# Kernel optimization log

Hardware: AMD Instinct MI355X
Metric: run time of the kernel (lower is better)

The kernel has to match this reference:

```python
import jax, jax.numpy as jnp
import numpy as np

EPS = 1e-8

def setup_inputs() -> dict:
    key = jax.random.key(0)
    k0, k1, k2, k3, k4 = jax.random.split(key, 5)
    B, N, K, Q, L, F = 8, 5, 5, 4, 128, 768
    support_emb = jax.random.normal(k0, (B, N, K, L, F), dtype=jnp.float32)
    query_emb = jax.random.normal(k1, (B, N * Q, L, F), dtype=jnp.float32)
    B_mask = jax.random.randint(k2, (B, N, K, L), 0, 2, dtype=jnp.int32)
    I_mask = jax.random.randint(k3, (B, N, K, L), 0, 2, dtype=jnp.int32)
    trigger_label = jax.random.randint(k4, (B, N * Q, L), 0, 2 * N + 1, dtype=jnp.int32)
    return {"support_emb": support_emb, "query_emb": query_emb, "B_mask": B_mask,
            "I_mask": I_mask, "trigger_label": trigger_label, "N": N, "K": K, "Q": Q}

def _proto(support_emb, Bm, Im, N):
    # support_emb: (B,N,K,L,F); Bm/Im: (B,N,K,L) float
    sum_B = jnp.einsum('bnklf,bnkl->bnf', support_emb, Bm)
    cnt_B = Bm.sum((2, 3))[..., None] + EPS
    pB = sum_B / cnt_B                                   # (B,N,F)
    sum_I = jnp.einsum('bnklf,bnkl->bnf', support_emb, Im)
    cnt_I = Im.sum((2, 3))[..., None] + EPS
    pI = sum_I / cnt_I                                   # (B,N,F)
    Om = 1.0 - Bm - Im                                   # (B,N,K,L)
    sum_O = jnp.einsum('bnklf,bnkl->bf', support_emb, Om)
    cnt_O = Om.sum((1, 2, 3))[:, None] + EPS
    pO = sum_O / cnt_O                                   # (B,F)
    Bsz, F = pO.shape
    # interleave: tags [O, B_0, I_0, B_1, I_1, ...]
    pBI = jnp.stack([pB, pI], axis=2).reshape(Bsz, 2 * N, F)
    return jnp.concatenate([pO[:, None, :], pBI], axis=1)  # (B, 2N+1, F)

def reference(support_emb, query_emb, B_mask, I_mask, trigger_label, N, K, Q):
    dt = support_emb.dtype
    Bm = B_mask.astype(dt)
    Im = I_mask.astype(dt)
    prototype = _proto(support_emb, Bm, Im, N)             # (B, 2N+1, F)
    # similarity: broadcast dot product -> batched GEMM
    logits = jnp.einsum('bqlf,btf->bqlt', query_emb, prototype)  # (B, NQ, L, 2N+1)
    T = logits.shape[-1]
    flat = logits.reshape(-1, T)
    pred = jnp.argmax(flat, axis=1)
    lab = trigger_label.reshape(-1)
    logp = jax.nn.log_softmax(flat, axis=-1)
    loss = -jnp.take_along_axis(logp, lab[:, None], axis=1).mean()
    return (loss, logits, pred)
```

## Files before the change

### kernel.cpp

```cpp
#include <hip/hip_runtime.h>
#include <cstdint>
#include <cstddef>

#define EPS 1e-8f

#define Bsz 8
#define Nn  5
#define Kk  5
#define Qq  4
#define Ll  128
#define Ff  768
#define NQ  (Nn*Qq)
#define Tt  (2*Nn+1)
#define KL  (Kk*Ll)
#define ROWS_PER_B (NQ*Ll)
#define NROWS (Bsz*ROWS_PER_B)
#define F4  (Ff/4)
#define BN  (Bsz*Nn)

#define S1_CHUNK 32
#define S1_CH    (KL / S1_CHUNK)

__global__ __launch_bounds__(256) void stage1_partials(
    const float* __restrict__ sup,
    const int*   __restrict__ Bm,
    const int*   __restrict__ Im,
    float* __restrict__ accum,
    float* __restrict__ cnt)
{
    int blk  = blockIdx.x;
    int bn   = blk / S1_CH;
    int ch   = blk - bn * S1_CH;
    int pos0 = ch * S1_CHUNK;
    int tid  = threadIdx.x;

    const float* sp = sup + ((size_t)bn * KL + pos0) * Ff;
    const int*   bp = Bm + bn * KL + pos0;
    const int*   ip = Im + bn * KL + pos0;

    __shared__ float smB[S1_CHUNK];
    __shared__ float smI[S1_CHUNK];
    if (tid < S1_CHUNK) {
        smB[tid] = (float)bp[tid];
        smI[tid] = (float)ip[tid];
    }
    __syncthreads();

    float aB0=0,aB1=0,aB2=0, aI0=0,aI1=0,aI2=0, aO0=0,aO1=0,aO2=0;
    const float* r = sp + tid;
    #pragma unroll 4
    for (int p = 0; p < S1_CHUNK; ++p, r += Ff) {
        float mb = smB[p], mi = smI[p];
        float mo = 1.0f - mb - mi;
        float v0 = r[0], v1 = r[256], v2 = r[512];
        aB0 = fmaf(mb, v0, aB0); aB1 = fmaf(mb, v1, aB1); aB2 = fmaf(mb, v2, aB2);
        aI0 = fmaf(mi, v0, aI0); aI1 = fmaf(mi, v1, aI1); aI2 = fmaf(mi, v2, aI2);
        aO0 = fmaf(mo, v0, aO0); aO1 = fmaf(mo, v1, aO1); aO2 = fmaf(mo, v2, aO2);
    }
    float* o = accum + (size_t)bn * (3 * Ff);
    atomicAdd(&o[tid],            aB0); atomicAdd(&o[tid + 256],          aB1); atomicAdd(&o[tid + 512],          aB2);
    atomicAdd(&o[Ff + tid],       aI0); atomicAdd(&o[Ff + tid + 256],     aI1); atomicAdd(&o[Ff + tid + 512],     aI2);
    atomicAdd(&o[2*Ff + tid],     aO0); atomicAdd(&o[2*Ff + tid + 256],   aO1); atomicAdd(&o[2*Ff + tid + 512],   aO2);

    if (tid == 0) { float c = 0; for (int p = 0; p < S1_CHUNK; ++p) c += smB[p]; atomicAdd(&cnt[bn*2],   c); }
    if (tid == 1) { float c = 0; for (int p = 0; p < S1_CHUNK; ++p) c += smI[p]; atomicAdd(&cnt[bn*2+1], c); }
}

__global__ void stage2_proto(
    const float* __restrict__ accum,
    const float* __restrict__ cnt,
    float* __restrict__ proto)
{
    int b = blockIdx.x;
    int f = threadIdx.x;

    float sumO = 0.0f, cntO = 0.0f;
    #pragma unroll
    for (int n = 0; n < Nn; ++n) {
        int bn = b * Nn + n;
        const float* a = accum + (size_t)bn * (3 * Ff);
        float cB = cnt[bn*2], cI = cnt[bn*2+1];
        proto[((size_t)b * Tt + (1 + 2 * n)) * Ff + f] = a[f]        / (cB + EPS);
        proto[((size_t)b * Tt + (2 + 2 * n)) * Ff + f] = a[Ff + f]   / (cI + EPS);
        sumO += a[2*Ff + f];
        cntO += (float)KL - cB - cI;
    }
    proto[(size_t)b * Tt * Ff + f] = sumO / (cntO + EPS);
}

#define S3_BLOCKS_PER_B 160
#define S3_ROWS_PER_WAVE 4

__global__ __launch_bounds__(256) void stage3_logits(
    const float* __restrict__ query,
    const float* __restrict__ proto,
    const int*   __restrict__ label,
    float* __restrict__ out_logits,
    float* __restrict__ out_pred,
    float* __restrict__ loss_out)
{
    __shared__ float sLoss;

    int b  = blockIdx.x / S3_BLOCKS_PER_B;
    int rg = blockIdx.x - b * S3_BLOCKS_PER_B;
    int wave = threadIdx.x >> 6;
    int lane = threadIdx.x & 63;

    if (threadIdx.x == 0) sLoss = 0.0f;
    __syncthreads();

    const float4* pg = (const float4*)(proto + (size_t)b * Tt * Ff);
    float4 P[Tt][3];
    #pragma unroll
    for (int t = 0; t < Tt; ++t) {
        P[t][0] = pg[t * F4 + lane];
        P[t][1] = pg[t * F4 + 64 + lane];
        P[t][2] = pg[t * F4 + 128 + lane];
    }

    int row0 = rg * (4 * S3_ROWS_PER_WAVE) + wave * S3_ROWS_PER_WAVE;
    float wloss = 0.0f;

    for (int r = 0; r < S3_ROWS_PER_WAVE; ++r) {
        size_t grow = (size_t)b * ROWS_PER_B + row0 + r;
        const float4* q = (const float4*)(query + grow * Ff);
        float4 q0 = q[lane], q1 = q[64 + lane], q2 = q[128 + lane];
        int lab = label[grow];

        float acc[Tt];
        #pragma unroll
        for (int t = 0; t < Tt; ++t) {
            float d;
            d = q0.x * P[t][0].x;
            d = fmaf(q0.y, P[t][0].y, d); d = fmaf(q0.z, P[t][0].z, d); d = fmaf(q0.w, P[t][0].w, d);
            d = fmaf(q1.x, P[t][1].x, d); d = fmaf(q1.y, P[t][1].y, d);
            d = fmaf(q1.z, P[t][1].z, d); d = fmaf(q1.w, P[t][1].w, d);
            d = fmaf(q2.x, P[t][2].x, d); d = fmaf(q2.y, P[t][2].y, d);
            d = fmaf(q2.z, P[t][2].z, d); d = fmaf(q2.w, P[t][2].w, d);
            acc[t] = d;
        }
        #pragma unroll
        for (int off = 32; off > 0; off >>= 1) {
            #pragma unroll
            for (int t = 0; t < Tt; ++t) acc[t] += __shfl_xor(acc[t], off, 64);
        }
        float m = acc[0]; int bt = 0;
        #pragma unroll
        for (int t = 1; t < Tt; ++t) if (acc[t] > m) { m = acc[t]; bt = t; }
        float s = 0.0f;
        #pragma unroll
        for (int t = 0; t < Tt; ++t) s += __expf(acc[t] - m);
        float labv = acc[0];
        #pragma unroll
        for (int t = 1; t < Tt; ++t) labv = (lab == t) ? acc[t] : labv;
        float myv = acc[0];
        #pragma unroll
        for (int t = 1; t < Tt; ++t) myv = (lane == t) ? acc[t] : myv;

        if (lane < Tt) out_logits[grow * Tt + lane] = myv;
        if (lane == 0) out_pred[grow] = (float)bt;
        wloss += (m + __logf(s)) - labv;
    }

    if (lane == 0) atomicAdd(&sLoss, wloss);
    __syncthreads();
    if (threadIdx.x == 0) atomicAdd(loss_out, sLoss * (1.0f / (float)NROWS));
}

extern "C" void kernel_launch(void* const* d_in, const int* in_sizes, int n_in,
                              void* d_out, int out_size, void* d_ws, size_t ws_size,
                              hipStream_t stream) {
    const float* sup   = (const float*)d_in[0];
    const float* query = (const float*)d_in[1];
    const int*   Bm    = (const int*)d_in[2];
    const int*   Im    = (const int*)d_in[3];
    const int*   lab   = (const int*)d_in[4];

    float* w     = (float*)d_ws;
    float* accum = w;
    float* cnt   = accum + (size_t)BN * 3 * Ff;
    float* proto = cnt + 2 * BN;
    size_t zeroBytes = ((size_t)BN * 3 * Ff + 2 * BN) * sizeof(float);

    float* loss_out   = (float*)d_out;
    float* out_logits = (float*)d_out + 1;
    float* out_pred   = (float*)d_out + 1 + (size_t)NROWS * Tt;

    hipMemsetAsync(d_ws, 0, zeroBytes, stream);
    hipMemsetAsync(d_out, 0, sizeof(float), stream);

    stage1_partials<<<BN * S1_CH, 256, 0, stream>>>(sup, Bm, Im, accum, cnt);
    stage2_proto<<<Bsz, Ff, 0, stream>>>(accum, cnt, proto);
    stage3_logits<<<Bsz * S3_BLOCKS_PER_B, 256, 0, stream>>>(query, proto, lab,
                                                             out_logits, out_pred, loss_out);
}
```

Measured before the change: 208.8 us.

## Fuse prototype normalization into logits kernel and vectorize support accumulation

Removes the separate stage2 prototype kernel. Each stage3 block now rebuilds its batch's prototypes in registers from the raw accumulators and counts, scaling by reciprocals. Stage1 switches to 192 threads with one float4 load per row instead of three strided scalar loads. This drops one kernel launch and the proto round trip through memory, at the cost of every stage3 block redundantly reading about 46KB of accumulators and doing the normalization again.

```diff
diff --git a/kernel.cpp b/kernel.cpp
--- a/kernel.cpp
+++ b/kernel.cpp
@@ -21,7 +21,7 @@
 #define S1_CHUNK 32
 #define S1_CH    (KL / S1_CHUNK)
 
-__global__ __launch_bounds__(256) void stage1_partials(
+__global__ __launch_bounds__(192) void stage1_partials(
     const float* __restrict__ sup,
     const int*   __restrict__ Bm,
     const int*   __restrict__ Im,
@@ -34,9 +34,9 @@
     int pos0 = ch * S1_CHUNK;
     int tid  = threadIdx.x;
 
-    const float* sp = sup + ((size_t)bn * KL + pos0) * Ff;
-    const int*   bp = Bm + bn * KL + pos0;
-    const int*   ip = Im + bn * KL + pos0;
+    const float4* sp = (const float4*)(sup + ((size_t)bn * KL + pos0) * Ff);
+    const int*    bp = Bm + bn * KL + pos0;
+    const int*    ip = Im + bn * KL + pos0;
 
     __shared__ float smB[S1_CHUNK];
     __shared__ float smI[S1_CHUNK];
@@ -46,46 +46,25 @@
     }
     __syncthreads();
 
-    float aB0=0,aB1=0,aB2=0, aI0=0,aI1=0,aI2=0, aO0=0,aO1=0,aO2=0;
-    const float* r = sp + tid;
+    float aBx=0,aBy=0,aBz=0,aBw=0, aIx=0,aIy=0,aIz=0,aIw=0, aOx=0,aOy=0,aOz=0,aOw=0;
+    const float4* r = sp + tid;
     #pragma unroll 4
-    for (int p = 0; p < S1_CHUNK; ++p, r += Ff) {
+    for (int p = 0; p < S1_CHUNK; ++p, r += F4) {
         float mb = smB[p], mi = smI[p];
         float mo = 1.0f - mb - mi;
-        float v0 = r[0], v1 = r[256], v2 = r[512];
-        aB0 = fmaf(mb, v0, aB0); aB1 = fmaf(mb, v1, aB1); aB2 = fmaf(mb, v2, aB2);
-        aI0 = fmaf(mi, v0, aI0); aI1 = fmaf(mi, v1, aI1); aI2 = fmaf(mi, v2, aI2);
-        aO0 = fmaf(mo, v0, aO0); aO1 = fmaf(mo, v1, aO1); aO2 = fmaf(mo, v2, aO2);
+        float4 v = *r;
+        aBx = fmaf(mb, v.x, aBx); aBy = fmaf(mb, v.y, aBy); aBz = fmaf(mb, v.z, aBz); aBw = fmaf(mb, v.w, aBw);
+        aIx = fmaf(mi, v.x, aIx); aIy = fmaf(mi, v.y, aIy); aIz = fmaf(mi, v.z, aIz); aIw = fmaf(mi, v.w, aIw);
+        aOx = fmaf(mo, v.x, aOx); aOy = fmaf(mo, v.y, aOy); aOz = fmaf(mo, v.z, aOz); aOw = fmaf(mo, v.w, aOw);
     }
     float* o = accum + (size_t)bn * (3 * Ff);
-    atomicAdd(&o[tid],            aB0); atomicAdd(&o[tid + 256],          aB1); atomicAdd(&o[tid + 512],          aB2);
-    atomicAdd(&o[Ff + tid],       aI0); atomicAdd(&o[Ff + tid + 256],     aI1); atomicAdd(&o[Ff + tid + 512],     aI2);
-    atomicAdd(&o[2*Ff + tid],     aO0); atomicAdd(&o[2*Ff + tid + 256],   aO1); atomicAdd(&o[2*Ff + tid + 512],   aO2);
+    int c = 4 * tid;
+    atomicAdd(&o[c],   aBx); atomicAdd(&o[c+1],   aBy); atomicAdd(&o[c+2],   aBz); atomicAdd(&o[c+3],   aBw);
+    atomicAdd(&o[Ff+c],aIx); atomicAdd(&o[Ff+c+1],aIy); atomicAdd(&o[Ff+c+2],aIz); atomicAdd(&o[Ff+c+3],aIw);
+    atomicAdd(&o[2*Ff+c],aOx); atomicAdd(&o[2*Ff+c+1],aOy); atomicAdd(&o[2*Ff+c+2],aOz); atomicAdd(&o[2*Ff+c+3],aOw);
 
-    if (tid == 0) { float c = 0; for (int p = 0; p < S1_CHUNK; ++p) c += smB[p]; atomicAdd(&cnt[bn*2],   c); }
-    if (tid == 1) { float c = 0; for (int p = 0; p < S1_CHUNK; ++p) c += smI[p]; atomicAdd(&cnt[bn*2+1], c); }
-}
-
-__global__ void stage2_proto(
-    const float* __restrict__ accum,
-    const float* __restrict__ cnt,
-    float* __restrict__ proto)
-{
-    int b = blockIdx.x;
-    int f = threadIdx.x;
-
-    float sumO = 0.0f, cntO = 0.0f;
-    #pragma unroll
-    for (int n = 0; n < Nn; ++n) {
-        int bn = b * Nn + n;
-        const float* a = accum + (size_t)bn * (3 * Ff);
-        float cB = cnt[bn*2], cI = cnt[bn*2+1];
-        proto[((size_t)b * Tt + (1 + 2 * n)) * Ff + f] = a[f]        / (cB + EPS);
-        proto[((size_t)b * Tt + (2 + 2 * n)) * Ff + f] = a[Ff + f]   / (cI + EPS);
-        sumO += a[2*Ff + f];
-        cntO += (float)KL - cB - cI;
-    }
-    proto[(size_t)b * Tt * Ff + f] = sumO / (cntO + EPS);
+    if (tid == 0) { float s = 0; for (int p = 0; p < S1_CHUNK; ++p) s += smB[p]; atomicAdd(&cnt[bn*2],   s); }
+    if (tid == 1) { float s = 0; for (int p = 0; p < S1_CHUNK; ++p) s += smI[p]; atomicAdd(&cnt[bn*2+1], s); }
 }
 
 #define S3_BLOCKS_PER_B 160
@@ -93,7 +72,8 @@
 
 __global__ __launch_bounds__(256) void stage3_logits(
     const float* __restrict__ query,
-    const float* __restrict__ proto,
+    const float* __restrict__ accum,
+    const float* __restrict__ cnt,
     const int*   __restrict__ label,
     float* __restrict__ out_logits,
     float* __restrict__ out_pred,
@@ -109,14 +89,33 @@
     if (threadIdx.x == 0) sLoss = 0.0f;
     __syncthreads();
 
-    const float4* pg = (const float4*)(proto + (size_t)b * Tt * Ff);
     float4 P[Tt][3];
+    float4 o0, o1, o2;
+    o0.x=o0.y=o0.z=o0.w=0; o1=o0; o2=o0;
+    float sumCB = 0.0f, sumCI = 0.0f;
     #pragma unroll
-    for (int t = 0; t < Tt; ++t) {
-        P[t][0] = pg[t * F4 + lane];
-        P[t][1] = pg[t * F4 + 64 + lane];
-        P[t][2] = pg[t * F4 + 128 + lane];
+    for (int n = 0; n < Nn; ++n) {
+        int bn = b * Nn + n;
+        const float4* a = (const float4*)(accum + (size_t)bn * (3 * Ff));
+        float cB = cnt[2*bn], cI = cnt[2*bn+1];
+        float sB = 1.0f / (cB + EPS);
+        float sI = 1.0f / (cI + EPS);
+        float4 v;
+        v = a[lane];            P[1+2*n][0].x=v.x*sB; P[1+2*n][0].y=v.y*sB; P[1+2*n][0].z=v.z*sB; P[1+2*n][0].w=v.w*sB;
+        v = a[64+lane];         P[1+2*n][1].x=v.x*sB; P[1+2*n][1].y=v.y*sB; P[1+2*n][1].z=v.z*sB; P[1+2*n][1].w=v.w*sB;
+        v = a[128+lane];        P[1+2*n][2].x=v.x*sB; P[1+2*n][2].y=v.y*sB; P[1+2*n][2].z=v.z*sB; P[1+2*n][2].w=v.w*sB;
+        v = a[192+lane];        P[2+2*n][0].x=v.x*sI; P[2+2*n][0].y=v.y*sI; P[2+2*n][0].z=v.z*sI; P[2+2*n][0].w=v.w*sI;
+        v = a[256+lane];        P[2+2*n][1].x=v.x*sI; P[2+2*n][1].y=v.y*sI; P[2+2*n][1].z=v.z*sI; P[2+2*n][1].w=v.w*sI;
+        v = a[320+lane];        P[2+2*n][2].x=v.x*sI; P[2+2*n][2].y=v.y*sI; P[2+2*n][2].z=v.z*sI; P[2+2*n][2].w=v.w*sI;
+        v = a[384+lane];        o0.x+=v.x; o0.y+=v.y; o0.z+=v.z; o0.w+=v.w;
+        v = a[448+lane];        o1.x+=v.x; o1.y+=v.y; o1.z+=v.z; o1.w+=v.w;
+        v = a[512+lane];        o2.x+=v.x; o2.y+=v.y; o2.z+=v.z; o2.w+=v.w;
+        sumCB += cB; sumCI += cI;
     }
+    float sO = 1.0f / ((float)(KL * Nn) - sumCB - sumCI + EPS);
+    P[0][0].x=o0.x*sO; P[0][0].y=o0.y*sO; P[0][0].z=o0.z*sO; P[0][0].w=o0.w*sO;
+    P[0][1].x=o1.x*sO; P[0][1].y=o1.y*sO; P[0][1].z=o1.z*sO; P[0][1].w=o1.w*sO;
+    P[0][2].x=o2.x*sO; P[0][2].y=o2.y*sO; P[0][2].z=o2.z*sO; P[0][2].w=o2.w*sO;
 
     int row0 = rg * (4 * S3_ROWS_PER_WAVE) + wave * S3_ROWS_PER_WAVE;
     float wloss = 0.0f;
@@ -179,7 +178,6 @@
     float* w     = (float*)d_ws;
     float* accum = w;
     float* cnt   = accum + (size_t)BN * 3 * Ff;
-    float* proto = cnt + 2 * BN;
     size_t zeroBytes = ((size_t)BN * 3 * Ff + 2 * BN) * sizeof(float);
 
     float* loss_out   = (float*)d_out;
@@ -189,8 +187,7 @@
     hipMemsetAsync(d_ws, 0, zeroBytes, stream);
     hipMemsetAsync(d_out, 0, sizeof(float), stream);
 
-    stage1_partials<<<BN * S1_CH, 256, 0, stream>>>(sup, Bm, Im, accum, cnt);
-    stage2_proto<<<Bsz, Ff, 0, stream>>>(accum, cnt, proto);
-    stage3_logits<<<Bsz * S3_BLOCKS_PER_B, 256, 0, stream>>>(query, proto, lab,
+    stage1_partials<<<BN * S1_CH, 192, 0, stream>>>(sup, Bm, Im, accum, cnt);
+    stage3_logits<<<Bsz * S3_BLOCKS_PER_B, 256, 0, stream>>>(query, accum, cnt, lab,
                                                              out_logits, out_pred, loss_out);
 }
```

After: 225.4 us. +7.9%, slower.
